# Kernel tuning notes

Measured on AMD Instinct MI355X. Metric: run time of the kernel, lower is better.

Reference implementation:

```python
import jax, jax.numpy as jnp
import numpy as np

S, B, NINP, NHID, NLAYERS = 512, 128, 128, 128, 3


def setup_inputs() -> dict:
    key = jax.random.key(0)
    ks = jax.random.split(key, 6)
    stdv = 1.0 / float(np.sqrt(NHID))
    u = lambda k, shape: jax.random.uniform(k, shape, jnp.float32, -stdv, stdv)
    return {
        "x": jax.random.normal(ks[0], (S, B, NINP), jnp.float32),
        "lin_w": u(ks[1], (NHID, NINP)),
        "lin_b": u(ks[2], (NHID,)),
        "W": u(ks[3], (NLAYERS, 4 * NHID, NHID)),
        "U": u(ks[4], (NLAYERS, 4 * NHID, NLAYERS * NHID)),
        "G": u(ks[5], (NLAYERS, NHID, 1)),
    }


def reference(x, lin_w, lin_b, W, U, G):
    # x: [S, B, ninp]; eval mode (no dropout masks), feedback=True, gated=True.
    S_, B_, _ = x.shape
    L = W.shape[0]
    H = W.shape[1] // 4
    xp = x @ lin_w.T + lin_b  # [S, B, H] input projection
    h0 = jnp.zeros((L, B_, H), x.dtype)
    c0 = jnp.zeros((L, B_, H), x.dtype)

    def step(carry, xt):
        h, c = carry  # each [L, B, H]
        # gated: per-layer scalar sigmoid gate, broadcast over H
        gh = jax.nn.sigmoid(jnp.einsum('lbh,lho->lbo', h, G))  # [L, B, 1]
        h = gh * h
        # feedback: concat all layers' hidden along features, shared by every layer
        hx = h.transpose(1, 0, 2).reshape(B_, L * H)  # [B, L*H]
        inp = xt  # [B, H]; stacked layers: output of layer i feeds layer i+1
        hs, cs = [], []
        for i in range(L):
            gates = inp @ W[i].T + hx @ U[i].T  # [B, 4H]
            ig, fg, gg, og = jnp.split(gates, 4, axis=-1)
            ig = jax.nn.sigmoid(ig)
            fg = jax.nn.sigmoid(fg)
            gg = jnp.tanh(gg)
            og = jax.nn.sigmoid(og)
            cy = fg * c[i] + ig * gg
            hy = og * jnp.tanh(cy)
            hs.append(hy)
            cs.append(cy)
            inp = hy
        return (jnp.stack(hs, 0), jnp.stack(cs, 0)), None

    (h, c), _ = jax.lax.scan(step, (h0, c0), xp)
    return (h, c)
```

## Files before the change

kernel.cpp:

```cpp
#include <hip/hip_runtime.h>

#define S_LEN 512
#define BATCH 128
#define NH    128
#define NL    3

#define HXS  392
#define INPS 136

#define XP_OFF   0u
#define WP_OFF   16777216u
#define UP_OFF   (WP_OFF + 393216u)
#define HX_OFF   (UP_OFF + 1179648u)
#define HX_SZ    294912u

typedef float f32x4 __attribute__((ext_vector_type(4)));
typedef short bf16x8 __attribute__((ext_vector_type(8)));
typedef unsigned u32x4 __attribute__((ext_vector_type(4)));
typedef unsigned long long u64;

__device__ __forceinline__ short f2bf(float f) {
    unsigned u = __builtin_bit_cast(unsigned, f);
    u = (u + 0x7FFFu + ((u >> 16) & 1u)) >> 16;
    return (short)u;
}
__device__ __forceinline__ float bf2f_lo(unsigned u) { return __builtin_bit_cast(float, u << 16); }
__device__ __forceinline__ float bf2f_hi(unsigned u) { return __builtin_bit_cast(float, u & 0xFFFF0000u); }
__device__ __forceinline__ float sigm(float x) { return 1.f / (1.f + __expf(-x)); }
__device__ __forceinline__ float tanh_fast(float x) { return 2.f / (1.f + __expf(-2.f * x)) - 1.f; }

__global__ __launch_bounds__(128) void xp_kernel(const float* __restrict__ x,
        const float* __restrict__ lin_w, const float* __restrict__ lin_b,
        short* __restrict__ xp) {
    __shared__ float xs[8 * 128];
    const int tid = threadIdx.x;
    const long r0 = (long)blockIdx.x * 8;
    for (int rr = 0; rr < 8; ++rr)
        xs[rr * 128 + tid] = x[(r0 + rr) * 128 + tid];
    __syncthreads();
    float acc[8];
    float bias = lin_b[tid];
    #pragma unroll
    for (int rr = 0; rr < 8; ++rr) acc[rr] = bias;
    const float* wrow = lin_w + (long)tid * 128;
    for (int k = 0; k < 128; ++k) {
        float wv = wrow[k];
        #pragma unroll
        for (int rr = 0; rr < 8; ++rr) acc[rr] += xs[rr * 128 + k] * wv;
    }
    for (int rr = 0; rr < 8; ++rr)
        xp[(r0 + rr) * 128 + tid] = f2bf(acc[rr]);
}

__global__ __launch_bounds__(256) void pack_kernel(const float* __restrict__ W,
        const float* __restrict__ U, short* __restrict__ Wp, short* __restrict__ Up) {
    int id = blockIdx.x * 256 + threadIdx.x;
    int lane = id & 63;
    int fid = id >> 6;
    int lr = lane & 15, lk = lane >> 4;
    if (fid < 384) {
        int kt = fid & 3, g = (fid >> 2) & 3, unit = fid >> 4;
        int l = unit >> 3, c = unit & 7;
        int row = g * 128 + c * 16 + lr;
        const float* src = W + ((long)(l * 512 + row)) * 128 + kt * 32 + lk * 8;
        short* dst = Wp + (long)fid * 512 + lane * 8;
        #pragma unroll
        for (int j = 0; j < 8; ++j) dst[j] = f2bf(src[j]);
    } else {
        int f = fid - 384;
        int kt = f % 12, gu = f / 12;
        int g = gu & 3, unit = gu >> 2;
        int l = unit >> 3, c = unit & 7;
        int row = g * 128 + c * 16 + lr;
        const float* src = U + ((long)(l * 512 + row)) * 384 + kt * 32 + lk * 8;
        short* dst = Up + (long)f * 512 + lane * 8;
        #pragma unroll
        for (int j = 0; j < 8; ++j) dst[j] = f2bf(src[j]);
    }
}


__global__ __launch_bounds__(256, 1) void lstm_kernel(
    const short* __restrict__ xp, const short* __restrict__ Wp,
    const short* __restrict__ Up, const float* __restrict__ Gp,
    char* __restrict__ hexch, float* __restrict__ out)
{
    __shared__ short hx_lds[16 * HXS];
    __shared__ short inp_lds[16 * INPS];
    __shared__ float gates_lds[4 * 16 * 17];
    __shared__ float G_lds[NL * 128];
    __shared__ short hsl[16 * 16];

    const int tid  = threadIdx.x;
    const int lane = tid & 63;
    const int w    = tid >> 6;
    const int lr   = lane & 15;
    const int lk   = lane >> 4;
    const int grp  = blockIdx.x & 7;
    const int unit = blockIdx.x >> 3;
    const int l    = unit >> 3;
    const int c    = unit & 7;
    const int b0   = grp * 16;
    const int bb   = tid >> 4;
    const int nn   = tid & 15;

    bf16x8 ufr[12], wfr[4];
    {
        const short* ub = Up + ((long)(unit * 4 + w) * 12) * 512 + lane * 8;
        #pragma unroll
        for (int kt = 0; kt < 12; ++kt) ufr[kt] = *(const bf16x8*)(ub + kt * 512);
        const short* wb = Wp + ((long)(unit * 4 + w) * 4) * 512 + lane * 8;
        #pragma unroll
        for (int kt = 0; kt < 4; ++kt) wfr[kt] = *(const bf16x8*)(wb + kt * 512);
    }
    #pragma unroll
    for (int kt = 0; kt < 12; ++kt) asm volatile("" : "+v"(ufr[kt]));
    #pragma unroll
    for (int kt = 0; kt < 4; ++kt)  asm volatile("" : "+v"(wfr[kt]));

    for (int i = tid; i < NL * 128; i += 256) G_lds[i] = Gp[i];
    float c_reg = 0.f;
    __syncthreads();

    const int offs[6] = {0, 6, 12, 16, 22, 28};
    const int nw[6]   = {3, 3, 2, 3, 3, 2};

    for (int t = 0; t < S_LEN; ++t) {
        const int par  = t & 1;
        const int ppar = par ^ 1;

        bf16x8 xa[4];
        if (l == 0) {
            const short* xp_t = xp + ((long)t * BATCH + b0) * 128;
            #pragma unroll
            for (int kt = 0; kt < 4; ++kt)
                xa[kt] = *(const bf16x8*)(xp_t + lr * 128 + kt * 32 + lk * 8);
        }

        if (t == 0) {
            for (int i = tid; i < 16 * HXS; i += 256) hx_lds[i] = 0;
        } else if (w < 3) {
            const int p = lane >> 2, sub = lane & 3;
            const unsigned want = (unsigned)t;
            const u64 abase = (u64)(hexch + (size_t)(((ppar * 8 + grp) * 3 + w)) * 6144
                                          + ((size_t)p * 24 + sub * 6) * 16);
            u32x4 q0, q1, q2, q3, q4, q5;
            for (int rounds = 0;; ++rounds) {
                asm volatile(
                    "global_load_dwordx4 %0, %6, off sc0 sc1\n\t"
                    "global_load_dwordx4 %1, %6, off offset:16 sc0 sc1\n\t"
                    "global_load_dwordx4 %2, %6, off offset:32 sc0 sc1\n\t"
                    "global_load_dwordx4 %3, %6, off offset:48 sc0 sc1\n\t"
                    "global_load_dwordx4 %4, %6, off offset:64 sc0 sc1\n\t"
                    "global_load_dwordx4 %5, %6, off offset:80 sc0 sc1\n\t"
                    "s_waitcnt vmcnt(0)"
                    : "=&v"(q0), "=&v"(q1), "=&v"(q2), "=&v"(q3), "=&v"(q4), "=&v"(q5)
                    : "v"(abase) : "memory");
                bool fresh = (q0[3] == want) && (q1[3] == want) && (q2[3] == want)
                          && (q3[3] == want) && (q4[3] == want) && (q5[3] == want);
                if (__all(fresh) || rounds > 262144) break;
            }
            const float* gb = &G_lds[w * 128 + sub * 32];
            float s = 0.f;
            u32x4 qs[6] = {q0, q1, q2, q3, q4, q5};
            #pragma unroll
            for (int k = 0; k < 6; ++k)
                #pragma unroll
                for (int i = 0; i < 3; ++i)
                    if (i < nw[k]) {
                        unsigned wd = qs[k][i];
                        s += bf2f_lo(wd) * gb[offs[k] + 2 * i]
                           + bf2f_hi(wd) * gb[offs[k] + 2 * i + 1];
                    }
            s += __shfl_xor(s, 1, 64);
            s += __shfl_xor(s, 2, 64);
            float gh = sigm(s);
            #pragma unroll
            for (int k = 0; k < 6; ++k)
                #pragma unroll
                for (int i = 0; i < 3; ++i)
                    if (i < nw[k]) {
                        unsigned wd = qs[k][i];
                        unsigned r = (unsigned)(unsigned short)f2bf(gh * bf2f_lo(wd))
                                   | ((unsigned)(unsigned short)f2bf(gh * bf2f_hi(wd)) << 16);
                        *(unsigned*)&hx_lds[p * HXS + w * 128 + sub * 32 + offs[k] + 2 * i] = r;
                    }
        }
        __syncthreads();

        f32x4 acc0 = (f32x4){0.f, 0.f, 0.f, 0.f};
        f32x4 acc1 = (f32x4){0.f, 0.f, 0.f, 0.f};
        #pragma unroll
        for (int kt = 0; kt < 12; ++kt) {
            bf16x8 a = *(const bf16x8*)&hx_lds[lr * HXS + kt * 32 + lk * 8];
            if (kt & 1) acc1 = __builtin_amdgcn_mfma_f32_16x16x32_bf16(a, ufr[kt], acc1, 0, 0, 0);
            else        acc0 = __builtin_amdgcn_mfma_f32_16x16x32_bf16(a, ufr[kt], acc0, 0, 0, 0);
        }

        if (l == 0) {
            #pragma unroll
            for (int kt = 0; kt < 4; ++kt) {
                if (kt & 1) acc1 = __builtin_amdgcn_mfma_f32_16x16x32_bf16(xa[kt], wfr[kt], acc1, 0, 0, 0);
                else        acc0 = __builtin_amdgcn_mfma_f32_16x16x32_bf16(xa[kt], wfr[kt], acc0, 0, 0, 0);
            }
        } else {
            const unsigned want = (unsigned)(t + 1);
            const u64 base = (u64)(hexch + (size_t)(((par * 8 + grp) * 3 + (l - 1))) * 6144);
            const int ch0 = tid;
            const u64 a0 = base + (size_t)ch0 * 16;
            const u64 a1 = a0 + 4096;
            u32x4 q0, q1;
            if (tid < 128) {
                for (int rounds = 0;; ++rounds) {
                    asm volatile(
                        "global_load_dwordx4 %0, %2, off sc0 sc1\n\t"
                        "global_load_dwordx4 %1, %3, off sc0 sc1\n\t"
                        "s_waitcnt vmcnt(0)"
                        : "=&v"(q0), "=&v"(q1) : "v"(a0), "v"(a1) : "memory");
                    if (__all((q0[3] == want) && (q1[3] == want)) || rounds > 262144) break;
                }
            } else {
                for (int rounds = 0;; ++rounds) {
                    asm volatile(
                        "global_load_dwordx4 %0, %1, off sc0 sc1\n\t"
                        "s_waitcnt vmcnt(0)"
                        : "=&v"(q0) : "v"(a0) : "memory");
                    if (__all(q0[3] == want) || rounds > 262144) break;
                }
            }
            {
                int row = ch0 / 24, m = ch0 % 24, cc = m / 3, j = m % 3;
                int sbase = row * INPS + cc * 16 + 6 * j;
                *(unsigned*)&inp_lds[sbase] = q0[0];
                *(unsigned*)&inp_lds[sbase + 2] = q0[1];
                if (j < 2) *(unsigned*)&inp_lds[sbase + 4] = q0[2];
                if (tid < 128) {
                    int ch1 = ch0 + 256;
                    int row1 = ch1 / 24, m1 = ch1 % 24, c1 = m1 / 3, j1 = m1 % 3;
                    int sb1 = row1 * INPS + c1 * 16 + 6 * j1;
                    *(unsigned*)&inp_lds[sb1] = q1[0];
                    *(unsigned*)&inp_lds[sb1 + 2] = q1[1];
                    if (j1 < 2) *(unsigned*)&inp_lds[sb1 + 4] = q1[2];
                }
            }
            __syncthreads();
            #pragma unroll
            for (int kt = 0; kt < 4; ++kt) {
                bf16x8 a = *(const bf16x8*)&inp_lds[lr * INPS + kt * 32 + lk * 8];
                if (kt & 1) acc1 = __builtin_amdgcn_mfma_f32_16x16x32_bf16(a, wfr[kt], acc1, 0, 0, 0);
                else        acc0 = __builtin_amdgcn_mfma_f32_16x16x32_bf16(a, wfr[kt], acc0, 0, 0, 0);
            }
        }

        #pragma unroll
        for (int r = 0; r < 4; ++r)
            gates_lds[w * 272 + (lk * 4 + r) * 17 + lr] = acc0[r] + acc1[r];
        __syncthreads();

        float ig = sigm(gates_lds[0 * 272 + bb * 17 + nn]);
        float fg = sigm(gates_lds[1 * 272 + bb * 17 + nn]);
        float gg = tanh_fast(gates_lds[2 * 272 + bb * 17 + nn]);
        float og = sigm(gates_lds[3 * 272 + bb * 17 + nn]);
        float cn = fg * c_reg + ig * gg;
        c_reg = cn;
        float hy = og * tanh_fast(cn);
        hsl[bb * 16 + nn] = f2bf(hy);
        if (t == S_LEN - 1) {
            long o = ((long)(l * BATCH + b0 + bb)) * NH + c * 16 + nn;
            out[o] = hy;
            out[(long)NL * BATCH * NH + o] = cn;
        }
        __syncthreads();

        if (tid < 48) {
            int row = tid / 3, j = tid % 3;
            const unsigned* hslw = (const unsigned*)hsl;
            unsigned d0, d1, d2;
            if (j < 2) { d0 = hslw[row * 8 + 3 * j]; d1 = hslw[row * 8 + 3 * j + 1]; d2 = hslw[row * 8 + 3 * j + 2]; }
            else       { d0 = hslw[row * 8 + 6];     d1 = hslw[row * 8 + 7];         d2 = 0; }
            u32x4 dq = (u32x4){d0, d1, d2, (unsigned)(t + 1)};
            u64 pa = (u64)(hexch + (size_t)(((par * 8 + grp) * 3 + l)) * 6144
                                 + ((size_t)row * 24 + c * 3 + j) * 16);
            asm volatile("global_store_dwordx4 %0, %1, off sc0 sc1" :: "v"(pa), "v"(dq) : "memory");
        }
    }
}

extern "C" void kernel_launch(void* const* d_in, const int* in_sizes, int n_in,
                              void* d_out, int out_size, void* d_ws, size_t ws_size,
                              hipStream_t stream) {
    const float* x     = (const float*)d_in[0];
    const float* lin_w = (const float*)d_in[1];
    const float* lin_b = (const float*)d_in[2];
    const float* W     = (const float*)d_in[3];
    const float* U     = (const float*)d_in[4];
    const float* G     = (const float*)d_in[5];
    float* out = (float*)d_out;

    short* xp    = (short*)((char*)d_ws + XP_OFF);
    short* Wp    = (short*)((char*)d_ws + WP_OFF);
    short* Up    = (short*)((char*)d_ws + UP_OFF);
    char*  hexch = (char*)d_ws + HX_OFF;

    hipMemsetAsync(hexch, 0, HX_SZ, stream);
    hipLaunchKernelGGL(xp_kernel,   dim3(8192), dim3(128), 0, stream, x, lin_w, lin_b, xp);
    hipLaunchKernelGGL(pack_kernel, dim3(384),  dim3(256), 0, stream, W, U, Wp, Up);
    hipLaunchKernelGGL(lstm_kernel, dim3(192),  dim3(256), 0, stream,
                       xp, Wp, Up, G, hexch, out);
}
```

Measured before the change: 4.058 ms.

## Overlap next-step layer 0/1 hidden feedback matmul with current step epilogue

Splits the recurrent U·hx product so the contributions from layers 0 and 1 for step t+1 are polled and computed at the end of step t, right after the cell update. Only layer 2's feedback is fetched at the top of the next step. The cell update and exchange store move from all 256 threads plus a staging LDS buffer to 48 lanes of one wave, each handling six columns and packing bf16 directly. This shortens the serial critical path between layers. In exchange it adds extra spin-waits and syncs on layers 0/1 data and concentrates the pointwise work on fewer lanes.

```diff
diff --git a/kernel.cpp b/kernel.cpp
--- a/kernel.cpp
+++ b/kernel.cpp
@@ -80,6 +80,18 @@
 }
 
 
+#define POLL6(q0,q1,q2,q3,q4,q5,ab) \
+    asm volatile( \
+        "global_load_dwordx4 %0, %6, off sc0 sc1\n\t" \
+        "global_load_dwordx4 %1, %6, off offset:16 sc0 sc1\n\t" \
+        "global_load_dwordx4 %2, %6, off offset:32 sc0 sc1\n\t" \
+        "global_load_dwordx4 %3, %6, off offset:48 sc0 sc1\n\t" \
+        "global_load_dwordx4 %4, %6, off offset:64 sc0 sc1\n\t" \
+        "global_load_dwordx4 %5, %6, off offset:80 sc0 sc1\n\t" \
+        "s_waitcnt vmcnt(0)" \
+        : "=&v"(q0), "=&v"(q1), "=&v"(q2), "=&v"(q3), "=&v"(q4), "=&v"(q5) \
+        : "v"(ab) : "memory")
+
 __global__ __launch_bounds__(256, 1) void lstm_kernel(
     const short* __restrict__ xp, const short* __restrict__ Wp,
     const short* __restrict__ Up, const float* __restrict__ Gp,
@@ -89,7 +101,6 @@
     __shared__ short inp_lds[16 * INPS];
     __shared__ float gates_lds[4 * 16 * 17];
     __shared__ float G_lds[NL * 128];
-    __shared__ short hsl[16 * 16];
 
     const int tid  = threadIdx.x;
     const int lane = tid & 63;
@@ -101,8 +112,6 @@
     const int l    = unit >> 3;
     const int c    = unit & 7;
     const int b0   = grp * 16;
-    const int bb   = tid >> 4;
-    const int nn   = tid & 15;
 
     bf16x8 ufr[12], wfr[4];
     {
@@ -119,15 +128,19 @@
     for (int kt = 0; kt < 4; ++kt)  asm volatile("" : "+v"(wfr[kt]));
 
     for (int i = tid; i < NL * 128; i += 256) G_lds[i] = Gp[i];
-    float c_reg = 0.f;
+    for (int i = tid; i < 16 * HXS; i += 256) hx_lds[i] = 0;
+    float c6[6] = {0.f, 0.f, 0.f, 0.f, 0.f, 0.f};
+    const int crow = lane / 3, cjj = lane % 3;
     __syncthreads();
 
     const int offs[6] = {0, 6, 12, 16, 22, 28};
     const int nw[6]   = {3, 3, 2, 3, 3, 2};
 
+    f32x4 acc0 = (f32x4){0.f, 0.f, 0.f, 0.f};
+    f32x4 acc1 = (f32x4){0.f, 0.f, 0.f, 0.f};
+
     for (int t = 0; t < S_LEN; ++t) {
-        const int par  = t & 1;
-        const int ppar = par ^ 1;
+        const int par = t & 1;
 
         bf16x8 xa[4];
         if (l == 0) {
@@ -137,30 +150,19 @@
                 xa[kt] = *(const bf16x8*)(xp_t + lr * 128 + kt * 32 + lk * 8);
         }
 
-        if (t == 0) {
-            for (int i = tid; i < 16 * HXS; i += 256) hx_lds[i] = 0;
-        } else if (w < 3) {
+        if (t > 0 && w == 2) {
             const int p = lane >> 2, sub = lane & 3;
             const unsigned want = (unsigned)t;
-            const u64 abase = (u64)(hexch + (size_t)(((ppar * 8 + grp) * 3 + w)) * 6144
+            const u64 abase = (u64)(hexch + (size_t)((((par ^ 1) * 8 + grp) * 3 + 2)) * 6144
                                           + ((size_t)p * 24 + sub * 6) * 16);
             u32x4 q0, q1, q2, q3, q4, q5;
             for (int rounds = 0;; ++rounds) {
-                asm volatile(
-                    "global_load_dwordx4 %0, %6, off sc0 sc1\n\t"
-                    "global_load_dwordx4 %1, %6, off offset:16 sc0 sc1\n\t"
-                    "global_load_dwordx4 %2, %6, off offset:32 sc0 sc1\n\t"
-                    "global_load_dwordx4 %3, %6, off offset:48 sc0 sc1\n\t"
-                    "global_load_dwordx4 %4, %6, off offset:64 sc0 sc1\n\t"
-                    "global_load_dwordx4 %5, %6, off offset:80 sc0 sc1\n\t"
-                    "s_waitcnt vmcnt(0)"
-                    : "=&v"(q0), "=&v"(q1), "=&v"(q2), "=&v"(q3), "=&v"(q4), "=&v"(q5)
-                    : "v"(abase) : "memory");
+                POLL6(q0, q1, q2, q3, q4, q5, abase);
                 bool fresh = (q0[3] == want) && (q1[3] == want) && (q2[3] == want)
                           && (q3[3] == want) && (q4[3] == want) && (q5[3] == want);
                 if (__all(fresh) || rounds > 262144) break;
             }
-            const float* gb = &G_lds[w * 128 + sub * 32];
+            const float* gb = &G_lds[2 * 128 + sub * 32];
             float s = 0.f;
             u32x4 qs[6] = {q0, q1, q2, q3, q4, q5};
             #pragma unroll
@@ -183,15 +185,13 @@
                         unsigned wd = qs[k][i];
                         unsigned r = (unsigned)(unsigned short)f2bf(gh * bf2f_lo(wd))
                                    | ((unsigned)(unsigned short)f2bf(gh * bf2f_hi(wd)) << 16);
-                        *(unsigned*)&hx_lds[p * HXS + w * 128 + sub * 32 + offs[k] + 2 * i] = r;
+                        *(unsigned*)&hx_lds[p * HXS + 2 * 128 + sub * 32 + offs[k] + 2 * i] = r;
                     }
         }
         __syncthreads();
 
-        f32x4 acc0 = (f32x4){0.f, 0.f, 0.f, 0.f};
-        f32x4 acc1 = (f32x4){0.f, 0.f, 0.f, 0.f};
-        #pragma unroll
-        for (int kt = 0; kt < 12; ++kt) {
+        #pragma unroll
+        for (int kt = 8; kt < 12; ++kt) {
             bf16x8 a = *(const bf16x8*)&hx_lds[lr * HXS + kt * 32 + lk * 8];
             if (kt & 1) acc1 = __builtin_amdgcn_mfma_f32_16x16x32_bf16(a, ufr[kt], acc1, 0, 0, 0);
             else        acc0 = __builtin_amdgcn_mfma_f32_16x16x32_bf16(a, ufr[kt], acc0, 0, 0, 0);
@@ -206,8 +206,7 @@
         } else {
             const unsigned want = (unsigned)(t + 1);
             const u64 base = (u64)(hexch + (size_t)(((par * 8 + grp) * 3 + (l - 1))) * 6144);
-            const int ch0 = tid;
-            const u64 a0 = base + (size_t)ch0 * 16;
+            const u64 a0 = base + (size_t)tid * 16;
             const u64 a1 = a0 + 4096;
             u32x4 q0, q1;
             if (tid < 128) {
@@ -229,13 +228,13 @@
                 }
             }
             {
-                int row = ch0 / 24, m = ch0 % 24, cc = m / 3, j = m % 3;
+                int row = tid / 24, m = tid % 24, cc = m / 3, j = m % 3;
                 int sbase = row * INPS + cc * 16 + 6 * j;
                 *(unsigned*)&inp_lds[sbase] = q0[0];
                 *(unsigned*)&inp_lds[sbase + 2] = q0[1];
                 if (j < 2) *(unsigned*)&inp_lds[sbase + 4] = q0[2];
                 if (tid < 128) {
-                    int ch1 = ch0 + 256;
+                    int ch1 = tid + 256;
                     int row1 = ch1 / 24, m1 = ch1 % 24, c1 = m1 / 3, j1 = m1 % 3;
                     int sb1 = row1 * INPS + c1 * 16 + 6 * j1;
                     *(unsigned*)&inp_lds[sb1] = q1[0];
@@ -255,33 +254,87 @@
         #pragma unroll
         for (int r = 0; r < 4; ++r)
             gates_lds[w * 272 + (lk * 4 + r) * 17 + lr] = acc0[r] + acc1[r];
+        acc0 = (f32x4){0.f, 0.f, 0.f, 0.f};
+        acc1 = (f32x4){0.f, 0.f, 0.f, 0.f};
         __syncthreads();
 
-        float ig = sigm(gates_lds[0 * 272 + bb * 17 + nn]);
-        float fg = sigm(gates_lds[1 * 272 + bb * 17 + nn]);
-        float gg = tanh_fast(gates_lds[2 * 272 + bb * 17 + nn]);
-        float og = sigm(gates_lds[3 * 272 + bb * 17 + nn]);
-        float cn = fg * c_reg + ig * gg;
-        c_reg = cn;
-        float hy = og * tanh_fast(cn);
-        hsl[bb * 16 + nn] = f2bf(hy);
-        if (t == S_LEN - 1) {
-            long o = ((long)(l * BATCH + b0 + bb)) * NH + c * 16 + nn;
-            out[o] = hy;
-            out[(long)NL * BATCH * NH + o] = cn;
-        }
-        __syncthreads();
-
-        if (tid < 48) {
-            int row = tid / 3, j = tid % 3;
-            const unsigned* hslw = (const unsigned*)hsl;
-            unsigned d0, d1, d2;
-            if (j < 2) { d0 = hslw[row * 8 + 3 * j]; d1 = hslw[row * 8 + 3 * j + 1]; d2 = hslw[row * 8 + 3 * j + 2]; }
-            else       { d0 = hslw[row * 8 + 6];     d1 = hslw[row * 8 + 7];         d2 = 0; }
-            u32x4 dq = (u32x4){d0, d1, d2, (unsigned)(t + 1)};
+        if (w == 3 && lane < 48) {
+            const int nv = (cjj == 2) ? 4 : 6;
+            unsigned dw0 = 0, dw1 = 0, dw2 = 0;
+            #pragma unroll
+            for (int k = 0; k < 6; ++k) {
+                if (k < nv) {
+                    int col = cjj * 6 + k;
+                    float ig = sigm(gates_lds[0 * 272 + crow * 17 + col]);
+                    float fg = sigm(gates_lds[1 * 272 + crow * 17 + col]);
+                    float gg = tanh_fast(gates_lds[2 * 272 + crow * 17 + col]);
+                    float og = sigm(gates_lds[3 * 272 + crow * 17 + col]);
+                    float cn = fg * c6[k] + ig * gg;
+                    c6[k] = cn;
+                    float hy = og * tanh_fast(cn);
+                    unsigned hb = (unsigned)(unsigned short)f2bf(hy) << ((k & 1) * 16);
+                    if (k < 2)      dw0 |= hb;
+                    else if (k < 4) dw1 |= hb;
+                    else            dw2 |= hb;
+                    if (t == S_LEN - 1) {
+                        long o = ((long)(l * BATCH + b0 + crow)) * NH + c * 16 + col;
+                        out[o] = hy;
+                        out[(long)NL * BATCH * NH + o] = cn;
+                    }
+                }
+            }
+            u32x4 dq = (u32x4){dw0, dw1, dw2, (unsigned)(t + 1)};
             u64 pa = (u64)(hexch + (size_t)(((par * 8 + grp) * 3 + l)) * 6144
-                                 + ((size_t)row * 24 + c * 3 + j) * 16);
+                                 + ((size_t)crow * 24 + c * 3 + cjj) * 16);
             asm volatile("global_store_dwordx4 %0, %1, off sc0 sc1" :: "v"(pa), "v"(dq) : "memory");
+        }
+
+        if (t < S_LEN - 1) {
+            if (w < 2) {
+                const int p = lane >> 2, sub = lane & 3;
+                const unsigned want = (unsigned)(t + 1);
+                const u64 abase = (u64)(hexch + (size_t)(((par * 8 + grp) * 3 + w)) * 6144
+                                              + ((size_t)p * 24 + sub * 6) * 16);
+                u32x4 q0, q1, q2, q3, q4, q5;
+                for (int rounds = 0;; ++rounds) {
+                    POLL6(q0, q1, q2, q3, q4, q5, abase);
+                    bool fresh = (q0[3] == want) && (q1[3] == want) && (q2[3] == want)
+                              && (q3[3] == want) && (q4[3] == want) && (q5[3] == want);
+                    if (__all(fresh) || rounds > 262144) break;
+                }
+                const float* gb = &G_lds[w * 128 + sub * 32];
+                float s = 0.f;
+                u32x4 qs[6] = {q0, q1, q2, q3, q4, q5};
+                #pragma unroll
+                for (int k = 0; k < 6; ++k)
+                    #pragma unroll
+                    for (int i = 0; i < 3; ++i)
+                        if (i < nw[k]) {
+                            unsigned wd = qs[k][i];
+                            s += bf2f_lo(wd) * gb[offs[k] + 2 * i]
+                               + bf2f_hi(wd) * gb[offs[k] + 2 * i + 1];
+                        }
+                s += __shfl_xor(s, 1, 64);
+                s += __shfl_xor(s, 2, 64);
+                float gh = sigm(s);
+                #pragma unroll
+                for (int k = 0; k < 6; ++k)
+                    #pragma unroll
+                    for (int i = 0; i < 3; ++i)
+                        if (i < nw[k]) {
+                            unsigned wd = qs[k][i];
+                            unsigned r = (unsigned)(unsigned short)f2bf(gh * bf2f_lo(wd))
+                                       | ((unsigned)(unsigned short)f2bf(gh * bf2f_hi(wd)) << 16);
+                            *(unsigned*)&hx_lds[p * HXS + w * 128 + sub * 32 + offs[k] + 2 * i] = r;
+                        }
+            }
+            __syncthreads();
+            #pragma unroll
+            for (int kt = 0; kt < 8; ++kt) {
+                bf16x8 a = *(const bf16x8*)&hx_lds[lr * HXS + kt * 32 + lk * 8];
+                if (kt & 1) acc1 = __builtin_amdgcn_mfma_f32_16x16x32_bf16(a, ufr[kt], acc1, 0, 0, 0);
+                else        acc0 = __builtin_amdgcn_mfma_f32_16x16x32_bf16(a, ufr[kt], acc0, 0, 0, 0);
+            }
         }
     }
 }
```

New measurement: 6.205 ms. 1.53x slower.

## Interleave gate rows per wave and overlap layer-2 hidden fetch with MFMA

Applied to the files above, without the earlier changes.

The W/U packing now interleaves the four gate rows inside each wave's 16-row MFMA tile. Each wave can then finish the LSTM cell in registers with lane shuffles, which removes the gates LDS round trip and two block barriers per step. The hidden-state exchange layout becomes column-major, one 16-byte record per column and 4-row group. Waves 0–1 fetch and gate layers 0–1 while wave 3 fetches layer 2 after the barrier, and an LDS flag lets the first 8 K-tiles of MFMA start before that third slice arrives. The cost is a larger exchange buffer, more spin-waiting, and more complex intra-block synchronization.

```diff
diff --git a/kernel.cpp b/kernel.cpp
--- a/kernel.cpp
+++ b/kernel.cpp
@@ -12,7 +12,7 @@
 #define WP_OFF   16777216u
 #define UP_OFF   (WP_OFF + 393216u)
 #define HX_OFF   (UP_OFF + 1179648u)
-#define HX_SZ    294912u
+#define HX_SZ    393216u
 
 typedef float f32x4 __attribute__((ext_vector_type(4)));
 typedef short bf16x8 __attribute__((ext_vector_type(8)));
@@ -26,6 +26,10 @@
 }
 __device__ __forceinline__ float bf2f_lo(unsigned u) { return __builtin_bit_cast(float, u << 16); }
 __device__ __forceinline__ float bf2f_hi(unsigned u) { return __builtin_bit_cast(float, u & 0xFFFF0000u); }
+__device__ __forceinline__ float chf(const u32x4& q, int r) {
+    unsigned wd = (r < 2) ? q[0] : q[1];
+    return (r & 1) ? bf2f_hi(wd) : bf2f_lo(wd);
+}
 __device__ __forceinline__ float sigm(float x) { return 1.f / (1.f + __expf(-x)); }
 __device__ __forceinline__ float tanh_fast(float x) { return 2.f / (1.f + __expf(-2.f * x)) - 1.f; }
 
@@ -57,11 +61,11 @@
     int id = blockIdx.x * 256 + threadIdx.x;
     int lane = id & 63;
     int fid = id >> 6;
-    int lr = lane & 15, lk = lane >> 4;
+    int n = lane & 15, lk = lane >> 4;
     if (fid < 384) {
-        int kt = fid & 3, g = (fid >> 2) & 3, unit = fid >> 4;
+        int kt = fid & 3, w = (fid >> 2) & 3, unit = fid >> 4;
         int l = unit >> 3, c = unit & 7;
-        int row = g * 128 + c * 16 + lr;
+        int row = (n >> 2) * 128 + c * 16 + w * 4 + (n & 3);
         const float* src = W + ((long)(l * 512 + row)) * 128 + kt * 32 + lk * 8;
         short* dst = Wp + (long)fid * 512 + lane * 8;
         #pragma unroll
@@ -69,9 +73,9 @@
     } else {
         int f = fid - 384;
         int kt = f % 12, gu = f / 12;
-        int g = gu & 3, unit = gu >> 2;
+        int w = gu & 3, unit = gu >> 2;
         int l = unit >> 3, c = unit & 7;
-        int row = g * 128 + c * 16 + lr;
+        int row = (n >> 2) * 128 + c * 16 + w * 4 + (n & 3);
         const float* src = U + ((long)(l * 512 + row)) * 384 + kt * 32 + lk * 8;
         short* dst = Up + (long)f * 512 + lane * 8;
         #pragma unroll
@@ -87,9 +91,8 @@
 {
     __shared__ short hx_lds[16 * HXS];
     __shared__ short inp_lds[16 * INPS];
-    __shared__ float gates_lds[4 * 16 * 17];
     __shared__ float G_lds[NL * 128];
-    __shared__ short hsl[16 * 16];
+    __shared__ unsigned hxflag;
 
     const int tid  = threadIdx.x;
     const int lane = tid & 63;
@@ -101,8 +104,6 @@
     const int l    = unit >> 3;
     const int c    = unit & 7;
     const int b0   = grp * 16;
-    const int bb   = tid >> 4;
-    const int nn   = tid & 15;
 
     bf16x8 ufr[12], wfr[4];
     {
@@ -119,15 +120,14 @@
     for (int kt = 0; kt < 4; ++kt)  asm volatile("" : "+v"(wfr[kt]));
 
     for (int i = tid; i < NL * 128; i += 256) G_lds[i] = Gp[i];
-    float c_reg = 0.f;
+    for (int i = tid; i < 16 * HXS; i += 256) hx_lds[i] = 0;
+    if (tid == 0) hxflag = 0;
+    float c_reg[4] = {0.f, 0.f, 0.f, 0.f};
     __syncthreads();
 
-    const int offs[6] = {0, 6, 12, 16, 22, 28};
-    const int nw[6]   = {3, 3, 2, 3, 3, 2};
-
     for (int t = 0; t < S_LEN; ++t) {
-        const int par  = t & 1;
-        const int ppar = par ^ 1;
+        const int par = t & 1;
+        __syncthreads();
 
         bf16x8 xa[4];
         if (l == 0) {
@@ -137,65 +137,129 @@
                 xa[kt] = *(const bf16x8*)(xp_t + lr * 128 + kt * 32 + lk * 8);
         }
 
-        if (t == 0) {
-            for (int i = tid; i < 16 * HXS; i += 256) hx_lds[i] = 0;
-        } else if (w < 3) {
-            const int p = lane >> 2, sub = lane & 3;
+        const int rg = lane >> 4, cg = lane & 15;
+        if (t > 0 && w < 2) {
             const unsigned want = (unsigned)t;
-            const u64 abase = (u64)(hexch + (size_t)(((ppar * 8 + grp) * 3 + w)) * 6144
-                                          + ((size_t)p * 24 + sub * 6) * 16);
-            u32x4 q0, q1, q2, q3, q4, q5;
+            const u64 ab = (u64)(hexch + (size_t)((((par ^ 1) * 8 + grp) * 3 + w)) * 8192
+                                       + (size_t)cg * 512 + (size_t)rg * 16);
+            u32x4 q0, q1, q2, q3, q4, q5, q6, q7;
             for (int rounds = 0;; ++rounds) {
                 asm volatile(
-                    "global_load_dwordx4 %0, %6, off sc0 sc1\n\t"
-                    "global_load_dwordx4 %1, %6, off offset:16 sc0 sc1\n\t"
-                    "global_load_dwordx4 %2, %6, off offset:32 sc0 sc1\n\t"
-                    "global_load_dwordx4 %3, %6, off offset:48 sc0 sc1\n\t"
-                    "global_load_dwordx4 %4, %6, off offset:64 sc0 sc1\n\t"
-                    "global_load_dwordx4 %5, %6, off offset:80 sc0 sc1\n\t"
+                    "global_load_dwordx4 %0, %8, off sc0 sc1\n\t"
+                    "global_load_dwordx4 %1, %8, off offset:64 sc0 sc1\n\t"
+                    "global_load_dwordx4 %2, %8, off offset:128 sc0 sc1\n\t"
+                    "global_load_dwordx4 %3, %8, off offset:192 sc0 sc1\n\t"
+                    "global_load_dwordx4 %4, %8, off offset:256 sc0 sc1\n\t"
+                    "global_load_dwordx4 %5, %8, off offset:320 sc0 sc1\n\t"
+                    "global_load_dwordx4 %6, %8, off offset:384 sc0 sc1\n\t"
+                    "global_load_dwordx4 %7, %8, off offset:448 sc0 sc1\n\t"
                     "s_waitcnt vmcnt(0)"
-                    : "=&v"(q0), "=&v"(q1), "=&v"(q2), "=&v"(q3), "=&v"(q4), "=&v"(q5)
-                    : "v"(abase) : "memory");
-                bool fresh = (q0[3] == want) && (q1[3] == want) && (q2[3] == want)
-                          && (q3[3] == want) && (q4[3] == want) && (q5[3] == want);
-                if (__all(fresh) || rounds > 262144) break;
-            }
-            const float* gb = &G_lds[w * 128 + sub * 32];
-            float s = 0.f;
-            u32x4 qs[6] = {q0, q1, q2, q3, q4, q5};
-            #pragma unroll
-            for (int k = 0; k < 6; ++k)
-                #pragma unroll
-                for (int i = 0; i < 3; ++i)
-                    if (i < nw[k]) {
-                        unsigned wd = qs[k][i];
-                        s += bf2f_lo(wd) * gb[offs[k] + 2 * i]
-                           + bf2f_hi(wd) * gb[offs[k] + 2 * i + 1];
-                    }
-            s += __shfl_xor(s, 1, 64);
-            s += __shfl_xor(s, 2, 64);
-            float gh = sigm(s);
-            #pragma unroll
-            for (int k = 0; k < 6; ++k)
-                #pragma unroll
-                for (int i = 0; i < 3; ++i)
-                    if (i < nw[k]) {
-                        unsigned wd = qs[k][i];
-                        unsigned r = (unsigned)(unsigned short)f2bf(gh * bf2f_lo(wd))
-                                   | ((unsigned)(unsigned short)f2bf(gh * bf2f_hi(wd)) << 16);
-                        *(unsigned*)&hx_lds[p * HXS + w * 128 + sub * 32 + offs[k] + 2 * i] = r;
-                    }
+                    : "=&v"(q0), "=&v"(q1), "=&v"(q2), "=&v"(q3),
+                      "=&v"(q4), "=&v"(q5), "=&v"(q6), "=&v"(q7)
+                    : "v"(ab) : "memory");
+                bool fr = (q0[3] == want) && (q1[3] == want) && (q2[3] == want) && (q3[3] == want)
+                       && (q4[3] == want) && (q5[3] == want) && (q6[3] == want) && (q7[3] == want);
+                if (__all(fr) || rounds > 262144) break;
+            }
+            u32x4 qs[8] = {q0, q1, q2, q3, q4, q5, q6, q7};
+            const float* gb = &G_lds[w * 128 + cg * 8];
+            float s[4] = {0.f, 0.f, 0.f, 0.f};
+            #pragma unroll
+            for (int k = 0; k < 8; ++k) {
+                float gk = gb[k];
+                #pragma unroll
+                for (int r = 0; r < 4; ++r) s[r] += chf(qs[k], r) * gk;
+            }
+            #pragma unroll
+            for (int m = 1; m <= 8; m <<= 1)
+                #pragma unroll
+                for (int r = 0; r < 4; ++r) s[r] += __shfl_xor(s[r], m, 64);
+            #pragma unroll
+            for (int r = 0; r < 4; ++r) {
+                float gh = sigm(s[r]);
+                unsigned wd[4];
+                #pragma unroll
+                for (int jj = 0; jj < 4; ++jj)
+                    wd[jj] = (unsigned)(unsigned short)f2bf(gh * chf(qs[2 * jj], r))
+                           | ((unsigned)(unsigned short)f2bf(gh * chf(qs[2 * jj + 1], r)) << 16);
+                *(u32x4*)&hx_lds[(rg * 4 + r) * HXS + w * 128 + cg * 8] =
+                    (u32x4){wd[0], wd[1], wd[2], wd[3]};
+            }
         }
         __syncthreads();
+
+        if (t > 0 && w == 3) {
+            const unsigned want = (unsigned)t;
+            const u64 ab = (u64)(hexch + (size_t)((((par ^ 1) * 8 + grp) * 3 + 2)) * 8192
+                                       + (size_t)cg * 512 + (size_t)rg * 16);
+            u32x4 q0, q1, q2, q3, q4, q5, q6, q7;
+            for (int rounds = 0;; ++rounds) {
+                asm volatile(
+                    "global_load_dwordx4 %0, %8, off sc0 sc1\n\t"
+                    "global_load_dwordx4 %1, %8, off offset:64 sc0 sc1\n\t"
+                    "global_load_dwordx4 %2, %8, off offset:128 sc0 sc1\n\t"
+                    "global_load_dwordx4 %3, %8, off offset:192 sc0 sc1\n\t"
+                    "global_load_dwordx4 %4, %8, off offset:256 sc0 sc1\n\t"
+                    "global_load_dwordx4 %5, %8, off offset:320 sc0 sc1\n\t"
+                    "global_load_dwordx4 %6, %8, off offset:384 sc0 sc1\n\t"
+                    "global_load_dwordx4 %7, %8, off offset:448 sc0 sc1\n\t"
+                    "s_waitcnt vmcnt(0)"
+                    : "=&v"(q0), "=&v"(q1), "=&v"(q2), "=&v"(q3),
+                      "=&v"(q4), "=&v"(q5), "=&v"(q6), "=&v"(q7)
+                    : "v"(ab) : "memory");
+                bool fr = (q0[3] == want) && (q1[3] == want) && (q2[3] == want) && (q3[3] == want)
+                       && (q4[3] == want) && (q5[3] == want) && (q6[3] == want) && (q7[3] == want);
+                if (__all(fr) || rounds > 262144) break;
+            }
+            u32x4 qs[8] = {q0, q1, q2, q3, q4, q5, q6, q7};
+            const float* gb = &G_lds[2 * 128 + cg * 8];
+            float s[4] = {0.f, 0.f, 0.f, 0.f};
+            #pragma unroll
+            for (int k = 0; k < 8; ++k) {
+                float gk = gb[k];
+                #pragma unroll
+                for (int r = 0; r < 4; ++r) s[r] += chf(qs[k], r) * gk;
+            }
+            #pragma unroll
+            for (int m = 1; m <= 8; m <<= 1)
+                #pragma unroll
+                for (int r = 0; r < 4; ++r) s[r] += __shfl_xor(s[r], m, 64);
+            #pragma unroll
+            for (int r = 0; r < 4; ++r) {
+                float gh = sigm(s[r]);
+                unsigned wd[4];
+                #pragma unroll
+                for (int jj = 0; jj < 4; ++jj)
+                    wd[jj] = (unsigned)(unsigned short)f2bf(gh * chf(qs[2 * jj], r))
+                           | ((unsigned)(unsigned short)f2bf(gh * chf(qs[2 * jj + 1], r)) << 16);
+                *(u32x4*)&hx_lds[(rg * 4 + r) * HXS + 2 * 128 + cg * 8] =
+                    (u32x4){wd[0], wd[1], wd[2], wd[3]};
+            }
+            if (lane == 0)
+                __hip_atomic_store(&hxflag, (unsigned)t, __ATOMIC_RELEASE, __HIP_MEMORY_SCOPE_WORKGROUP);
+        }
 
         f32x4 acc0 = (f32x4){0.f, 0.f, 0.f, 0.f};
         f32x4 acc1 = (f32x4){0.f, 0.f, 0.f, 0.f};
         #pragma unroll
-        for (int kt = 0; kt < 12; ++kt) {
+        for (int kt = 0; kt < 8; ++kt) {
             bf16x8 a = *(const bf16x8*)&hx_lds[lr * HXS + kt * 32 + lk * 8];
             if (kt & 1) acc1 = __builtin_amdgcn_mfma_f32_16x16x32_bf16(a, ufr[kt], acc1, 0, 0, 0);
             else        acc0 = __builtin_amdgcn_mfma_f32_16x16x32_bf16(a, ufr[kt], acc0, 0, 0, 0);
         }
+        if (t > 0) {
+            int guard = 0;
+            while (__hip_atomic_load(&hxflag, __ATOMIC_ACQUIRE, __HIP_MEMORY_SCOPE_WORKGROUP)
+                   < (unsigned)t) {
+                if (++guard > 40000000) break;
+            }
+        }
+        #pragma unroll
+        for (int kt = 8; kt < 12; ++kt) {
+            bf16x8 a = *(const bf16x8*)&hx_lds[lr * HXS + kt * 32 + lk * 8];
+            if (kt & 1) acc1 = __builtin_amdgcn_mfma_f32_16x16x32_bf16(a, ufr[kt], acc1, 0, 0, 0);
+            else        acc0 = __builtin_amdgcn_mfma_f32_16x16x32_bf16(a, ufr[kt], acc0, 0, 0, 0);
+        }
 
         if (l == 0) {
             #pragma unroll
@@ -205,43 +269,29 @@
             }
         } else {
             const unsigned want = (unsigned)(t + 1);
-            const u64 base = (u64)(hexch + (size_t)(((par * 8 + grp) * 3 + (l - 1))) * 6144);
-            const int ch0 = tid;
-            const u64 a0 = base + (size_t)ch0 * 16;
+            const u64 base = (u64)(hexch + (size_t)(((par * 8 + grp) * 3 + (l - 1))) * 8192);
+            const u64 a0 = base + (size_t)tid * 16;
             const u64 a1 = a0 + 4096;
             u32x4 q0, q1;
-            if (tid < 128) {
-                for (int rounds = 0;; ++rounds) {
-                    asm volatile(
-                        "global_load_dwordx4 %0, %2, off sc0 sc1\n\t"
-                        "global_load_dwordx4 %1, %3, off sc0 sc1\n\t"
-                        "s_waitcnt vmcnt(0)"
-                        : "=&v"(q0), "=&v"(q1) : "v"(a0), "v"(a1) : "memory");
-                    if (__all((q0[3] == want) && (q1[3] == want)) || rounds > 262144) break;
-                }
-            } else {
-                for (int rounds = 0;; ++rounds) {
-                    asm volatile(
-                        "global_load_dwordx4 %0, %1, off sc0 sc1\n\t"
-                        "s_waitcnt vmcnt(0)"
-                        : "=&v"(q0) : "v"(a0) : "memory");
-                    if (__all(q0[3] == want) || rounds > 262144) break;
-                }
+            for (int rounds = 0;; ++rounds) {
+                asm volatile(
+                    "global_load_dwordx4 %0, %2, off sc0 sc1\n\t"
+                    "global_load_dwordx4 %1, %3, off sc0 sc1\n\t"
+                    "s_waitcnt vmcnt(0)"
+                    : "=&v"(q0), "=&v"(q1) : "v"(a0), "v"(a1) : "memory");
+                if (__all((q0[3] == want) && (q1[3] == want)) || rounds > 262144) break;
             }
             {
-                int row = ch0 / 24, m = ch0 % 24, cc = m / 3, j = m % 3;
-                int sbase = row * INPS + cc * 16 + 6 * j;
-                *(unsigned*)&inp_lds[sbase] = q0[0];
-                *(unsigned*)&inp_lds[sbase + 2] = q0[1];
-                if (j < 2) *(unsigned*)&inp_lds[sbase + 4] = q0[2];
-                if (tid < 128) {
-                    int ch1 = ch0 + 256;
-                    int row1 = ch1 / 24, m1 = ch1 % 24, c1 = m1 / 3, j1 = m1 % 3;
-                    int sb1 = row1 * INPS + c1 * 16 + 6 * j1;
-                    *(unsigned*)&inp_lds[sb1] = q1[0];
-                    *(unsigned*)&inp_lds[sb1 + 2] = q1[1];
-                    if (j1 < 2) *(unsigned*)&inp_lds[sb1 + 4] = q1[2];
-                }
+                int col0 = tid >> 2, rg0 = tid & 3;
+                inp_lds[(rg0 * 4 + 0) * INPS + col0] = (short)(q0[0] & 0xffff);
+                inp_lds[(rg0 * 4 + 1) * INPS + col0] = (short)(q0[0] >> 16);
+                inp_lds[(rg0 * 4 + 2) * INPS + col0] = (short)(q0[1] & 0xffff);
+                inp_lds[(rg0 * 4 + 3) * INPS + col0] = (short)(q0[1] >> 16);
+                int m1 = tid + 256, col1 = m1 >> 2, rg1 = m1 & 3;
+                inp_lds[(rg1 * 4 + 0) * INPS + col1] = (short)(q1[0] & 0xffff);
+                inp_lds[(rg1 * 4 + 1) * INPS + col1] = (short)(q1[0] >> 16);
+                inp_lds[(rg1 * 4 + 2) * INPS + col1] = (short)(q1[1] & 0xffff);
+                inp_lds[(rg1 * 4 + 3) * INPS + col1] = (short)(q1[1] >> 16);
             }
             __syncthreads();
             #pragma unroll
@@ -252,36 +302,45 @@
             }
         }
 
-        #pragma unroll
-        for (int r = 0; r < 4; ++r)
-            gates_lds[w * 272 + (lk * 4 + r) * 17 + lr] = acc0[r] + acc1[r];
-        __syncthreads();
-
-        float ig = sigm(gates_lds[0 * 272 + bb * 17 + nn]);
-        float fg = sigm(gates_lds[1 * 272 + bb * 17 + nn]);
-        float gg = tanh_fast(gates_lds[2 * 272 + bb * 17 + nn]);
-        float og = sigm(gates_lds[3 * 272 + bb * 17 + nn]);
-        float cn = fg * c_reg + ig * gg;
-        c_reg = cn;
-        float hy = og * tanh_fast(cn);
-        hsl[bb * 16 + nn] = f2bf(hy);
-        if (t == S_LEN - 1) {
-            long o = ((long)(l * BATCH + b0 + bb)) * NH + c * 16 + nn;
-            out[o] = hy;
-            out[(long)NL * BATCH * NH + o] = cn;
-        }
-        __syncthreads();
-
-        if (tid < 48) {
-            int row = tid / 3, j = tid % 3;
-            const unsigned* hslw = (const unsigned*)hsl;
-            unsigned d0, d1, d2;
-            if (j < 2) { d0 = hslw[row * 8 + 3 * j]; d1 = hslw[row * 8 + 3 * j + 1]; d2 = hslw[row * 8 + 3 * j + 2]; }
-            else       { d0 = hslw[row * 8 + 6];     d1 = hslw[row * 8 + 7];         d2 = 0; }
-            u32x4 dq = (u32x4){d0, d1, d2, (unsigned)(t + 1)};
-            u64 pa = (u64)(hexch + (size_t)(((par * 8 + grp) * 3 + l)) * 6144
-                                 + ((size_t)row * 24 + c * 3 + j) * 16);
+        f32x4 ac = acc0 + acc1;
+        f32x4 vf, vg, vo;
+        #pragma unroll
+        for (int r = 0; r < 4; ++r) {
+            vf[r] = __shfl_xor(ac[r], 4, 64);
+            vg[r] = __shfl_xor(ac[r], 8, 64);
+            vo[r] = __shfl_xor(ac[r], 12, 64);
+        }
+        if (lr < 4) {
+            unsigned hw[2];
+            float hys[4], cns[4];
+            #pragma unroll
+            for (int r = 0; r < 4; ++r) {
+                float ig = sigm(ac[r]);
+                float fg = sigm(vf[r]);
+                float gg = tanh_fast(vg[r]);
+                float og = sigm(vo[r]);
+                float cn = fg * c_reg[r] + ig * gg;
+                c_reg[r] = cn;
+                cns[r] = cn;
+                hys[r] = og * tanh_fast(cn);
+            }
+            hw[0] = (unsigned)(unsigned short)f2bf(hys[0])
+                  | ((unsigned)(unsigned short)f2bf(hys[1]) << 16);
+            hw[1] = (unsigned)(unsigned short)f2bf(hys[2])
+                  | ((unsigned)(unsigned short)f2bf(hys[3]) << 16);
+            u32x4 dq = (u32x4){hw[0], hw[1], 0u, (unsigned)(t + 1)};
+            const int col = c * 16 + w * 4 + lr;
+            u64 pa = (u64)(hexch + (size_t)(((par * 8 + grp) * 3 + l)) * 8192
+                                 + ((size_t)col * 4 + lk) * 16);
             asm volatile("global_store_dwordx4 %0, %1, off sc0 sc1" :: "v"(pa), "v"(dq) : "memory");
+            if (t == S_LEN - 1) {
+                #pragma unroll
+                for (int r = 0; r < 4; ++r) {
+                    long o = ((long)(l * BATCH + b0 + lk * 4 + r)) * NH + col;
+                    out[o] = hys[r];
+                    out[(long)NL * BATCH * NH + o] = cns[r];
+                }
+            }
         }
     }
 }
@@ -302,7 +361,7 @@
     short* Up    = (short*)((char*)d_ws + UP_OFF);
     char*  hexch = (char*)d_ws + HX_OFF;
 
-    hipMemsetAsync(hexch, 0, HX_SZ, stream);
+    (void)hipMemsetAsync(hexch, 0, HX_SZ, stream);
     hipLaunchKernelGGL(xp_kernel,   dim3(8192), dim3(128), 0, stream, x, lin_w, lin_b, xp);
     hipLaunchKernelGGL(pack_kernel, dim3(384),  dim3(256), 0, stream, W, U, Wp, Up);
     hipLaunchKernelGGL(lstm_kernel, dim3(192),  dim3(256), 0, stream,
```

Result: faster. 3.295 ms (median of 2 runs) (-18.8%).
